# Performance work log

Measured on AMD Instinct MI355X. Metric: run time of the kernel, lower is better.

The kernel has to match this reference:

```python
import jax, jax.numpy as jnp
import numpy as np

E = 100   # embed_size
H = 64    # q_hidden_num
B, T, K = 64, 20, 50
I, U = 50000, 10000


def setup_inputs() -> dict:
    key = jax.random.key(0)
    ks = jax.random.split(key, 16)
    # sample_vectors: table = sigma[i]*randn + mu[i]; sigma=[1,1,1,.1,.1,1,1], mu=0
    alpha = jax.random.normal(ks[0], (I, E), jnp.float32)
    rho = jax.random.normal(ks[1], (I, E), jnp.float32)
    lam = jax.random.normal(ks[2], (I, E), jnp.float32)
    beta = 0.1 * jax.random.normal(ks[3], (I, E), jnp.float32)
    mu_tab = 0.1 * jax.random.normal(ks[4], (I, E), jnp.float32)
    theta = jax.random.normal(ks[5], (U, E), jnp.float32)
    gamma = jax.random.normal(ks[6], (U, E), jnp.float32)
    w1 = jax.random.normal(ks[7], (H, E), jnp.float32) / np.sqrt(E)
    b1 = jnp.zeros((H,), jnp.float32)
    w2 = jax.random.normal(ks[8], (1, H), jnp.float32) / np.sqrt(H)
    b2 = jnp.zeros((1,), jnp.float32)
    sigma_list = jnp.array([1.0, 1.0, 1.0, 0.1, 0.1, 1.0, 1.0], jnp.float32)
    mu_list = jnp.zeros((7,), jnp.float32)
    prices = jax.random.uniform(ks[9], (B, T), jnp.float32, 1.0, 20.0)
    price_table = jax.random.uniform(ks[10], (I,), jnp.float32, 1.0, 20.0)
    item_ids = jax.random.randint(ks[11], (B, T), 0, I, jnp.int32)
    # distinct itemset ids per row (contiguous random window)
    starts = jax.random.randint(ks[12], (B,), 0, I - K, jnp.int32)
    itemset = starts[:, None] + jnp.arange(K, dtype=jnp.int32)[None, :]
    userid = jax.random.randint(ks[13], (B,), 0, U, jnp.int32)
    return dict(alpha=alpha, rho=rho, lam=lam, beta=beta, mu_tab=mu_tab,
                theta=theta, gamma=gamma, w1=w1, b1=b1, w2=w2, b2=b2,
                sigma_list=sigma_list, mu_list=mu_list, prices=prices,
                price_table=price_table, item_ids=item_ids, itemset=itemset,
                userid=userid, batch_size=B)


def reference(alpha, rho, lam, beta, mu_tab, theta, gamma, w1, b1, w2, b2,
              sigma_list, mu_list, prices, price_table, item_ids, itemset,
              userid, batch_size):
    f32 = alpha.dtype

    def Qf(x):  # Q_function in eval mode (dropout identity)
        h = jax.nn.relu(x @ w1.T + b1)
        return jax.nn.sigmoid(h @ w2.T + b2)  # [..., 1]; mean over last dim == itself

    def prior_sum(v, idx):  # sum_e 0.5*(v-mu)*(-(v-mu)/sigma)
        return (-0.5 / sigma_list[idx]) * jnp.sum((v - mu_list[idx]) ** 2)

    th = theta[userid]   # [B,E]
    ga = gamma[userid]   # [B,E]
    a_c = alpha[itemset]; r_c = rho[itemset]; l_c = lam[itemset]
    b_c = beta[itemset]; m_c = mu_tab[itemset]          # [B,K,E]
    a0 = alpha[item_ids]; r0 = rho[item_ids]
    l0 = lam[item_ids]; b0 = beta[item_ids]             # [B,T,E]

    # ---- f prior ----
    q_l = (Qf(a_c).sum() + Qf(r_c).sum() + Qf(l_c).sum() + Qf(b_c).sum()
           + Qf(m_c).sum() + Qf(th).sum() + Qf(ga).sum())
    p_l = (prior_sum(a_c, 0) + prior_sum(r_c, 1) + prior_sum(l_c, 2)
           + prior_sum(b_c, 3) + prior_sum(m_c, 4)
           + prior_sum(th, 5) + prior_sum(ga, 6))

    # ---- kesai(item, user, price) ----
    def kes(a_i, b_i, l_i, th_b, ga_b, price):
        return (l_i.mean(-1) + (th_b * a_i).mean(-1)
                - (ga_b * b_i).mean(-1) * jnp.log(price))

    kes0 = kes(a0, b0, l0, th[:, None, :], ga[:, None, :], prices)            # [B,T]
    kesc = kes(a_c, b_c, l_c, th[:, None, :], ga[:, None, :], price_table[itemset])  # [B,K]

    # list-aliasing bug: basket at step k = [item0, c_0..c_k] (c_j skipped iff ==item0)
    m = itemset[:, None, :] != item_ids[:, :, None]     # [B,T,K]
    mf = m.astype(f32)
    S = a0[:, :, None, :] + jnp.cumsum(mf[..., None] * a_c[:, None, :, :], axis=2)  # [B,T,K,E]
    lenk = 1.0 + jnp.cumsum(mf, axis=2)                 # [B,T,K]

    D = jnp.einsum('btke,bje->btkj', S, r_c)            # rho_cj . S_k
    rda0 = jnp.einsum('bje,bte->btj', r_c, a0)          # rho_cj . alpha_item0
    A_kj = jnp.einsum('bke,bje->bkj', a_c, r_c)         # rho_cj . alpha_ck

    denom = (lenk + 1.0)[..., None] * E                 # [B,T,K,1]
    j_gt_k = jnp.arange(K)[:, None] < jnp.arange(K)[None, :]
    elig = m[:, :, None, :] & j_gt_k[None, None, :, :]  # [B,T,K,K]
    NEG = jnp.asarray(-1e30, f32)

    val0 = (D + rda0[:, :, None, :]) / denom + kesc[:, None, None, :]
    look0 = jnp.maximum(0.0, jnp.max(jnp.where(elig, val0, NEG), axis=-1))
    valc = (D + A_kj[:, None, :, :]) / denom + kesc[:, None, None, :]
    lookc = jnp.maximum(0.0, jnp.max(jnp.where(elig, valc, NEG), axis=-1))

    interact0 = jnp.einsum('bte,btke->btk', r0, S) / (E * lenk)
    interactc = jnp.einsum('bke,btke->btk', r_c, S) / (E * lenk)

    Kes0 = kes0[:, :, None] + interact0 + look0
    KesC = kesc[:, None, :] + interactc + lookc
    basket = jnp.sum(jnp.where(m, jax.nn.log_sigmoid(Kes0 - KesC), 0.0))

    # torch: loss = sum over batch; torch.mean(scalar) == scalar
    return p_l - q_l + basket
```

## Files before the change

### kernel.cpp

```cpp
#include <hip/hip_runtime.h>
#include <math.h>

#define Ee 100
#define Hh 64
#define Bb 64
#define Tt 20
#define Kk 50
#define NROWS (5*Bb*Kk + 2*Bb)
#define NQUADS (NROWS/4)
#define PREBLKS 256
#define QBLKS   512
#define NB3 (Bb*Tt)

__device__ __forceinline__ float wave_sum(float v) {
    #pragma unroll
    for (int m = 32; m >= 1; m >>= 1) v += __shfl_xor(v, m, 64);
    return v;
}
__device__ __forceinline__ float rl(float v, int l) {
    return __uint_as_float(__builtin_amdgcn_readlane(__float_as_uint(v), l));
}

__global__ __launch_bounds__(256) void k_fused1(
    const float* __restrict__ alpha, const float* __restrict__ rho,
    const float* __restrict__ lam,   const float* __restrict__ beta,
    const float* __restrict__ mu_tab,const float* __restrict__ theta,
    const float* __restrict__ gamma_,const float* __restrict__ w1,
    const float* __restrict__ b1,    const float* __restrict__ w2,
    const float* __restrict__ b2,    const float* __restrict__ sigma_list,
    const float* __restrict__ prices,const float* __restrict__ price_table,
    const int* __restrict__ item_ids,const int* __restrict__ itemset,
    const int* __restrict__ userid,
    float* __restrict__ A, float* __restrict__ rda0, float* __restrict__ ra0c,
    float* __restrict__ kesc, float* __restrict__ kes0, float* __restrict__ rda0self,
    float* __restrict__ partialQ)
{
    __shared__ float buf[12224];
    const int lane = threadIdx.x & 63;
    const int wid  = threadIdx.x >> 6;

    if (blockIdx.x < PREBLKS) {
        float* acT = buf;
        float* rcT = buf + 5200;
        float* a0T = buf + 10400;
        float* r0T = buf + 11200;
        float* th  = buf + 12000;
        float* ga  = buf + 12100;

        const int b = blockIdx.x >> 2, q = blockIdx.x & 3;
        const int kcnt = (q < 2) ? 13 : 12;
        const int kbeg = q*12 + ((q < 2) ? q : 2);
        const int tbeg = q*5;
        const long uid = userid[b];

        for (int i = threadIdx.x; i < Ee; i += 256) {
            th[i] = theta[uid*Ee+i];
            ga[i] = gamma_[uid*Ee+i];
        }
        for (int i = threadIdx.x; i < 2500; i += 256) {
            int ii = (i < 1250) ? i : i - 1250;
            int k = ii % 50, c = ii / 50;
            long idx = itemset[b*Kk+k];
            const float* src = ((i < 1250) ? alpha : rho) + idx*Ee + 4*c;
            float4 v = *(const float4*)src;
            float* dst = (i < 1250) ? acT : rcT;
            dst[(4*c+0)*52+k] = v.x; dst[(4*c+1)*52+k] = v.y;
            dst[(4*c+2)*52+k] = v.z; dst[(4*c+3)*52+k] = v.w;
        }
        for (int i = threadIdx.x; i < 250; i += 256) {
            int ii = (i < 125) ? i : i - 125;
            int tl = ii % 5, c = ii / 5;
            long idx = item_ids[b*Tt + tbeg + tl];
            const float* src = ((i < 125) ? alpha : rho) + idx*Ee + 4*c;
            float4 v = *(const float4*)src;
            float* dst = (i < 125) ? a0T : r0T;
            dst[(4*c+0)*8+tl] = v.x; dst[(4*c+1)*8+tl] = v.y;
            dst[(4*c+2)*8+tl] = v.z; dst[(4*c+3)*8+tl] = v.w;
        }
        __syncthreads();

        const int tid = threadIdx.x;
        if (tid < kcnt*13) {
            int k = kbeg + tid/13, jt = tid - (tid/13)*13, j0 = 4*jt;
            float s0=0.f, s1=0.f, s2=0.f, s3=0.f;
            #pragma unroll 4
            for (int e = 0; e < Ee; ++e) {
                float a  = acT[e*52 + k];
                float4 r = *(const float4*)&rcT[e*52 + j0];
                s0 = fmaf(a, r.x, s0); s1 = fmaf(a, r.y, s1);
                s2 = fmaf(a, r.z, s2); s3 = fmaf(a, r.w, s3);
            }
            float* dst = A + ((long)b*Kk + k)*Kk + j0;
            dst[0] = s0; dst[1] = s1;
            if (jt < 12) { dst[2] = s2; dst[3] = s3; }
        } else if (tid < kcnt*13 + 65) {
            int t2 = tid - kcnt*13;
            int tl = t2/13, jt = t2 - tl*13, j0 = 4*jt;
            float p0=0.f,p1=0.f,p2=0.f,p3=0.f, q0=0.f,q1=0.f,q2=0.f,q3=0.f;
            #pragma unroll 4
            for (int e = 0; e < Ee; ++e) {
                float a0v = a0T[e*8 + tl];
                float r0v = r0T[e*8 + tl];
                float4 r = *(const float4*)&rcT[e*52 + j0];
                float4 a = *(const float4*)&acT[e*52 + j0];
                p0 = fmaf(r.x, a0v, p0); p1 = fmaf(r.y, a0v, p1);
                p2 = fmaf(r.z, a0v, p2); p3 = fmaf(r.w, a0v, p3);
                q0 = fmaf(r0v, a.x, q0); q1 = fmaf(r0v, a.y, q1);
                q2 = fmaf(r0v, a.z, q2); q3 = fmaf(r0v, a.w, q3);
            }
            int t = tbeg + tl;
            float* d1 = rda0 + ((long)b*Tt + t)*Kk + j0;
            float* d2 = ra0c + ((long)b*Tt + t)*Kk + j0;
            d1[0]=p0; d1[1]=p1; d2[0]=q0; d2[1]=q1;
            if (jt < 12) { d1[2]=p2; d1[3]=p3; d2[2]=q2; d2[3]=q3; }
        }

        for (int task = wid; task < 5 + kcnt; task += 4) {
            if (task < 5) {
                int tl = task, t = tbeg + tl;
                long idx = item_ids[b*Tt+t];
                float s=0.f, ml=0.f, mtha=0.f, mgb=0.f;
                if (lane < Kk) {
                    #pragma unroll
                    for (int u = 0; u < 2; ++u) {
                        int e = lane + u*Kk;
                        float a0v = a0T[e*8+tl], r0v = r0T[e*8+tl];
                        s    = fmaf(r0v, a0v, s);
                        ml  += lam[idx*Ee+e];
                        mtha = fmaf(th[e], a0v, mtha);
                        mgb  = fmaf(ga[e], beta[idx*Ee+e], mgb);
                    }
                }
                s = wave_sum(s); ml = wave_sum(ml); mtha = wave_sum(mtha); mgb = wave_sum(mgb);
                if (lane == 0) {
                    rda0self[b*Tt+t] = s;
                    kes0[b*Tt+t] = 0.01f*ml + 0.01f*mtha - 0.01f*mgb*logf(prices[b*Tt+t]);
                }
            } else {
                int k = kbeg + (task - 5);
                long idx = itemset[b*Kk+k];
                float ml=0.f, mtha=0.f, mgb=0.f;
                if (lane < Kk) {
                    #pragma unroll
                    for (int u = 0; u < 2; ++u) {
                        int e = lane + u*Kk;
                        ml  += lam[idx*Ee+e];
                        mtha = fmaf(th[e], acT[e*52+k], mtha);
                        mgb  = fmaf(ga[e], beta[idx*Ee+e], mgb);
                    }
                }
                ml = wave_sum(ml); mtha = wave_sum(mtha); mgb = wave_sum(mgb);
                if (lane == 0)
                    kesc[b*Kk+k] = 0.01f*ml + 0.01f*mtha - 0.01f*mgb*logf(price_table[idx]);
            }
        }
    } else {
        float* w1s = buf;
        float* red = buf + 6400;

        for (int i = threadIdx.x; i < Hh*Ee/4; i += 256)
            *(float4*)&w1s[4*i] = *(const float4*)&w1[4*i];
        __syncthreads();

        const float w2j = w2[lane];
        const float b1j = b1[lane];
        const float b2v = b2[0];
        const float c0 = -0.5f/sigma_list[0], c1 = -0.5f/sigma_list[1];
        const float c2 = -0.5f/sigma_list[2], c3 = -0.5f/sigma_list[3];
        const float c4 = -0.5f/sigma_list[4], c5 = -0.5f/sigma_list[5];
        const float c6 = -0.5f/sigma_list[6];

        const bool ldA = (lane < 25);
        const bool ldB = (lane >= 32) && (lane < 57);
        const int  lq  = ldA ? (lane<<2) : ((lane-32)<<2);
        const int  wave = (blockIdx.x - PREBLKS)*4 + wid;

        #define LOAD_QUAD(Q, AB, CD, CF)                                          \
        {                                                                         \
            int r4_ = 4*(Q);                                                      \
            const float* tab_; int4 ii_;                                          \
            if (r4_ < 16000) {                                                    \
                int seg_ = r4_/3200;                                              \
                ii_ = *(const int4*)&itemset[r4_ - seg_*3200];                    \
                tab_ = (seg_==0)?alpha:(seg_==1)?rho:(seg_==2)?lam                \
                      :(seg_==3)?beta:mu_tab;                                     \
                CF = (seg_==0)?c0:(seg_==1)?c1:(seg_==2)?c2:(seg_==3)?c3:c4;      \
            } else if (r4_ < 16064) {                                             \
                ii_ = *(const int4*)&userid[r4_-16000]; tab_ = theta;  CF = c5;   \
            } else {                                                              \
                ii_ = *(const int4*)&userid[r4_-16064]; tab_ = gamma_; CF = c6;   \
            }                                                                     \
            if (ldA) {                                                            \
                AB = *(const float4*)(tab_ + (long)ii_.x*Ee + lq);                \
                CD = *(const float4*)(tab_ + (long)ii_.z*Ee + lq);                \
            } else if (ldB) {                                                     \
                AB = *(const float4*)(tab_ + (long)ii_.y*Ee + lq);                \
                CD = *(const float4*)(tab_ + (long)ii_.w*Ee + lq);                \
            }                                                                     \
        }

        float ssacc = 0.f;
        float qacc  = 0.f;
        float4 curAB = make_float4(0.f,0.f,0.f,0.f);
        float4 curCD = make_float4(0.f,0.f,0.f,0.f);
        float  ccur = 0.f;
        int qd = wave;
        if (qd < NQUADS) LOAD_QUAD(qd, curAB, curCD, ccur);

        while (qd < NQUADS) {
            float4 nAB = make_float4(0.f,0.f,0.f,0.f);
            float4 nCD = make_float4(0.f,0.f,0.f,0.f);
            float  cnx = 0.f;
            int qn = qd + QBLKS*4;
            if (qn < NQUADS) LOAD_QUAD(qn, nAB, nCD, cnx);

            if (ldA || ldB)
                ssacc += ccur * (curAB.x*curAB.x + curAB.y*curAB.y
                               + curAB.z*curAB.z + curAB.w*curAB.w
                               + curCD.x*curCD.x + curCD.y*curCD.y
                               + curCD.z*curCD.z + curCD.w*curCD.w);

            float hA0=b1j, hA1=0.f, hB0=b1j, hB1=0.f;
            float hC0=b1j, hC1=0.f, hD0=b1j, hD1=0.f;
            #pragma unroll
            for (int i = 0; i < 25; ++i) {
                float4 wv = *(const float4*)&w1s[lane*Ee + 4*i];
                hA0 = fmaf(rl(curAB.x, i),    wv.x, hA0);
                hA1 = fmaf(rl(curAB.y, i),    wv.y, hA1);
                hA0 = fmaf(rl(curAB.z, i),    wv.z, hA0);
                hA1 = fmaf(rl(curAB.w, i),    wv.w, hA1);
                hB0 = fmaf(rl(curAB.x, 32+i), wv.x, hB0);
                hB1 = fmaf(rl(curAB.y, 32+i), wv.y, hB1);
                hB0 = fmaf(rl(curAB.z, 32+i), wv.z, hB0);
                hB1 = fmaf(rl(curAB.w, 32+i), wv.w, hB1);
                hC0 = fmaf(rl(curCD.x, i),    wv.x, hC0);
                hC1 = fmaf(rl(curCD.y, i),    wv.y, hC1);
                hC0 = fmaf(rl(curCD.z, i),    wv.z, hC0);
                hC1 = fmaf(rl(curCD.w, i),    wv.w, hC1);
                hD0 = fmaf(rl(curCD.x, 32+i), wv.x, hD0);
                hD1 = fmaf(rl(curCD.y, 32+i), wv.y, hD1);
                hD0 = fmaf(rl(curCD.z, 32+i), wv.z, hD0);
                hD1 = fmaf(rl(curCD.w, 32+i), wv.w, hD1);
            }
            float vA = fmaxf(hA0+hA1, 0.f)*w2j;
            float vB = fmaxf(hB0+hB1, 0.f)*w2j;
            float vC = fmaxf(hC0+hC1, 0.f)*w2j;
            float vD = fmaxf(hD0+hD1, 0.f)*w2j;
            #pragma unroll
            for (int m = 32; m >= 1; m >>= 1) {
                vA += __shfl_xor(vA, m, 64);
                vB += __shfl_xor(vB, m, 64);
                vC += __shfl_xor(vC, m, 64);
                vD += __shfl_xor(vD, m, 64);
            }
            qacc -= 1.f/(1.f+expf(-(vA+b2v))) + 1.f/(1.f+expf(-(vB+b2v)))
                  + 1.f/(1.f+expf(-(vC+b2v))) + 1.f/(1.f+expf(-(vD+b2v)));

            curAB = nAB; curCD = nCD; ccur = cnx; qd = qn;
        }
        #undef LOAD_QUAD

        float s = wave_sum(ssacc);
        if (lane == 0) red[wid] = s + qacc;
        __syncthreads();
        if (threadIdx.x == 0)
            partialQ[blockIdx.x - PREBLKS] = red[0]+red[1]+red[2]+red[3];
    }
}

__global__ __launch_bounds__(64) void k_main(
    const float* __restrict__ A, const float* __restrict__ rda0,
    const float* __restrict__ ra0c, const float* __restrict__ kesc,
    const float* __restrict__ kes0, const float* __restrict__ rda0self,
    const int* __restrict__ item_ids, const int* __restrict__ itemset,
    float* __restrict__ partial)
{
    __shared__ float Als[Kk*51];
    __shared__ float Cum[Kk*51];
    __shared__ float2 js[Kk];

    const int bt = blockIdx.x;
    const int b  = bt / Tt;
    const int lane = threadIdx.x;

    for (int i = lane; i < Kk*Kk; i += 64) {
        int k = i / Kk;
        Als[k*51 + (i - k*Kk)] = A[(long)b*Kk*Kk + i];
    }

    const int  myitem = item_ids[bt];
    const bool valid  = lane < Kk;
    const int  cj     = valid ? itemset[b*Kk+lane] : -1;
    const bool mj     = valid && (cj != myitem);
    const unsigned long long mask = __ballot(mj);

    const float rj_own = valid ? rda0[(long)bt*Kk+lane] : 0.f;
    const float kc_own = valid ? kesc[b*Kk+lane] : 0.f;
    const float raj    = valid ? ra0c[(long)bt*Kk+lane] : 0.f;
    if (valid) js[lane] = make_float2(rj_own, kc_own);

    const unsigned mlo = (unsigned)mask, mhi = (unsigned)(mask >> 32);
    const int below = __builtin_amdgcn_mbcnt_hi(mhi, __builtin_amdgcn_mbcnt_lo(mlo, 0));
    const float len    = 1.f + (float)below + (mj ? 1.f : 0.f);
    const float invden = 1.f / ((len + 1.f) * (float)Ee);
    const float invlen = 1.f / ((float)Ee * len);

    float pv = mj ? raj : 0.f;
    #pragma unroll
    for (int off = 1; off <= 32; off <<= 1) {
        float u = __shfl_up(pv, off, 64);
        if (lane >= off) pv += u;
    }
    const float cumra  = pv;
    const float r0self = rda0self[bt];
    const float k0     = kes0[bt];

    asm volatile("s_waitcnt lgkmcnt(0)" ::: "memory");

    if (valid) {
        float cum = 0.f;
        #pragma unroll 5
        for (int k = 0; k < Kk; ++k) {
            float mfk = ((mask >> k) & 1ull) ? 1.0f : 0.0f;
            cum = fmaf(mfk, Als[k*51 + lane], cum);
            Cum[k*51 + lane] = cum;
        }
    }
    asm volatile("s_waitcnt lgkmcnt(0)" ::: "memory");

    const int lc = valid ? lane : (Kk-1);
    float max0 = -3e38f, maxc = -3e38f, diag = 0.f;
    #pragma unroll 2
    for (int j = 0; j < Kk; ++j) {
        float c = Cum[lc*51 + j];
        if (j == lane) diag = c;
        if ((mask >> j) & 1ull) {
            float  a  = Als[lc*51 + j];
            float2 sj = js[j];
            float v0 = fmaf(c + 2.f*sj.x, invden, sj.y);
            float vc = fmaf(a - sj.x,    invden, v0);
            if (lane < j) { max0 = fmaxf(max0, v0); maxc = fmaxf(maxc, vc); }
        }
    }

    float look0 = fmaxf(0.f, max0);
    float lookc = fmaxf(0.f, maxc);
    float Kes0 = k0     + fmaf(r0self + cumra, invlen, look0);
    float KesC = kc_own + fmaf(rj_own + diag,  invlen, lookc);
    float x = Kes0 - KesC;
    float term = (x >= 0.f) ? -log1pf(expf(-x)) : (x - log1pf(expf(x)));
    float contrib = mj ? term : 0.f;
    float s = wave_sum(contrib);
    if (lane == 0) partial[bt] = s;
}

__global__ __launch_bounds__(256) void k_final(
    const float* __restrict__ p1, int n1,
    const float* __restrict__ p3, int n3,
    float* __restrict__ out)
{
    __shared__ double sh[256];
    double s = 0.0;
    for (int i = threadIdx.x; i < n1; i += 256) s += (double)p1[i];
    for (int i = threadIdx.x; i < n3; i += 256) s += (double)p3[i];
    sh[threadIdx.x] = s;
    __syncthreads();
    for (int m = 128; m >= 1; m >>= 1) {
        if (threadIdx.x < m) sh[threadIdx.x] += sh[threadIdx.x + m];
        __syncthreads();
    }
    if (threadIdx.x == 0) out[0] = (float)sh[0];
}

extern "C" void kernel_launch(void* const* d_in, const int* in_sizes, int n_in,
                              void* d_out, int out_size, void* d_ws, size_t ws_size,
                              hipStream_t stream) {
    const float* alpha      = (const float*)d_in[0];
    const float* rho        = (const float*)d_in[1];
    const float* lam        = (const float*)d_in[2];
    const float* beta       = (const float*)d_in[3];
    const float* mu_tab     = (const float*)d_in[4];
    const float* theta      = (const float*)d_in[5];
    const float* gamma_     = (const float*)d_in[6];
    const float* w1         = (const float*)d_in[7];
    const float* b1         = (const float*)d_in[8];
    const float* w2         = (const float*)d_in[9];
    const float* b2         = (const float*)d_in[10];
    const float* sigma_list = (const float*)d_in[11];
    const float* prices      = (const float*)d_in[13];
    const float* price_table = (const float*)d_in[14];
    const int*   item_ids    = (const int*)d_in[15];
    const int*   itemset     = (const int*)d_in[16];
    const int*   userid      = (const int*)d_in[17];

    float* ws = (float*)d_ws;
    const size_t offA    = 0;
    const size_t offRDA  = offA   + (size_t)Bb*Kk*Kk;
    const size_t offRA0C = offRDA + (size_t)Bb*Tt*Kk;
    const size_t offKESC = offRA0C+ (size_t)Bb*Tt*Kk;
    const size_t offKES0 = offKESC+ (size_t)Bb*Kk;
    const size_t offSELF = offKES0+ (size_t)Bb*Tt;
    const size_t offP1   = offSELF+ (size_t)Bb*Tt;
    const size_t offP3   = offP1  + QBLKS;

    k_fused1<<<PREBLKS + QBLKS, 256, 0, stream>>>(
        alpha, rho, lam, beta, mu_tab, theta, gamma_,
        w1, b1, w2, b2, sigma_list, prices, price_table,
        item_ids, itemset, userid,
        ws + offA, ws + offRDA, ws + offRA0C,
        ws + offKESC, ws + offKES0, ws + offSELF,
        ws + offP1);
    k_main<<<NB3, 64, 0, stream>>>(ws + offA, ws + offRDA, ws + offRA0C,
                                   ws + offKESC, ws + offKES0, ws + offSELF,
                                   item_ids, itemset, ws + offP3);
    k_final<<<1, 256, 0, stream>>>(ws + offP1, QBLKS, ws + offP3, NB3, (float*)d_out);
}
```

Baseline: 36.41 us.

## Fuse basket stage into per-batch blocks, dropping k_main and global intermediates

```diff
diff --git a/kernel.cpp b/kernel.cpp
--- a/kernel.cpp
+++ b/kernel.cpp
@@ -6,11 +6,28 @@
 #define Bb 64
 #define Tt 20
 #define Kk 50
-#define NROWS (5*Bb*Kk + 2*Bb)
-#define NQUADS (NROWS/4)
-#define PREBLKS 256
-#define QBLKS   512
-#define NB3 (Bb*Tt)
+#define NROWS 16128
+#define NQUADS 4032
+#define BBLKS 64
+#define QBLKS 448
+#define NBLK (BBLKS + QBLKS)
+
+#define O_ACT   0
+#define O_RCT   5200
+#define O_P     5200
+#define O_W     7760
+#define O_ALS   10400
+#define O_RDA   12950
+#define O_RA0   13950
+#define O_KESC  14950
+#define O_KES0  15000
+#define O_SELF  15020
+#define O_TH    15040
+#define O_GA    15140
+#define O_IIS   15240
+#define O_IID   15292
+#define O_RED   15312
+#define LDSF    15320
 
 __device__ __forceinline__ float wave_sum(float v) {
     #pragma unroll
@@ -21,7 +38,7 @@
     return __uint_as_float(__builtin_amdgcn_readlane(__float_as_uint(v), l));
 }
 
-__global__ __launch_bounds__(256) void k_fused1(
+__global__ __launch_bounds__(256) void k_fused(
     const float* __restrict__ alpha, const float* __restrict__ rho,
     const float* __restrict__ lam,   const float* __restrict__ beta,
     const float* __restrict__ mu_tab,const float* __restrict__ theta,
@@ -31,134 +48,227 @@
     const float* __restrict__ prices,const float* __restrict__ price_table,
     const int* __restrict__ item_ids,const int* __restrict__ itemset,
     const int* __restrict__ userid,
-    float* __restrict__ A, float* __restrict__ rda0, float* __restrict__ ra0c,
-    float* __restrict__ kesc, float* __restrict__ kes0, float* __restrict__ rda0self,
-    float* __restrict__ partialQ)
+    float* __restrict__ partial)
 {
-    __shared__ float buf[12224];
-    const int lane = threadIdx.x & 63;
-    const int wid  = threadIdx.x >> 6;
-
-    if (blockIdx.x < PREBLKS) {
-        float* acT = buf;
-        float* rcT = buf + 5200;
-        float* a0T = buf + 10400;
-        float* r0T = buf + 11200;
-        float* th  = buf + 12000;
-        float* ga  = buf + 12100;
-
-        const int b = blockIdx.x >> 2, q = blockIdx.x & 3;
-        const int kcnt = (q < 2) ? 13 : 12;
-        const int kbeg = q*12 + ((q < 2) ? q : 2);
-        const int tbeg = q*5;
-        const long uid = userid[b];
-
-        for (int i = threadIdx.x; i < Ee; i += 256) {
-            th[i] = theta[uid*Ee+i];
-            ga[i] = gamma_[uid*Ee+i];
-        }
-        for (int i = threadIdx.x; i < 2500; i += 256) {
-            int ii = (i < 1250) ? i : i - 1250;
-            int k = ii % 50, c = ii / 50;
-            long idx = itemset[b*Kk+k];
-            const float* src = ((i < 1250) ? alpha : rho) + idx*Ee + 4*c;
-            float4 v = *(const float4*)src;
-            float* dst = (i < 1250) ? acT : rcT;
+    __shared__ float buf[LDSF];
+    const int tid  = threadIdx.x;
+    const int lane = tid & 63;
+    const int wid  = tid >> 6;
+
+    if (blockIdx.x < BBLKS) {
+        const int b = blockIdx.x;
+        int* iis = (int*)&buf[O_IIS];
+        int* iid = (int*)&buf[O_IID];
+
+        if (tid < Kk) iis[tid] = itemset[b*Kk + tid];
+        else if (tid < Kk + Tt) iid[tid - Kk] = item_ids[b*Tt + (tid - Kk)];
+        {
+            const long uid = userid[b];
+            if (tid >= 64 && tid < 89)
+                *(float4*)&buf[O_TH + 4*(tid-64)] = *(const float4*)&theta[uid*Ee + 4*(tid-64)];
+            else if (tid >= 96 && tid < 121)
+                *(float4*)&buf[O_GA + 4*(tid-96)] = *(const float4*)&gamma_[uid*Ee + 4*(tid-96)];
+        }
+        for (int i = tid; i < 2500; i += 256) {
+            int half = (i < 1250) ? 0 : 1;
+            int ii = i - half*1250;
+            int k = ii % Kk, c = ii / Kk;
+            long idx = itemset[b*Kk + k];
+            float4 v = *(const float4*)((half ? rho : alpha) + idx*Ee + 4*c);
+            float* dst = &buf[half ? O_RCT : O_ACT];
             dst[(4*c+0)*52+k] = v.x; dst[(4*c+1)*52+k] = v.y;
             dst[(4*c+2)*52+k] = v.z; dst[(4*c+3)*52+k] = v.w;
         }
-        for (int i = threadIdx.x; i < 250; i += 256) {
-            int ii = (i < 125) ? i : i - 125;
-            int tl = ii % 5, c = ii / 5;
-            long idx = item_ids[b*Tt + tbeg + tl];
-            const float* src = ((i < 125) ? alpha : rho) + idx*Ee + 4*c;
-            float4 v = *(const float4*)src;
-            float* dst = (i < 125) ? a0T : r0T;
-            dst[(4*c+0)*8+tl] = v.x; dst[(4*c+1)*8+tl] = v.y;
-            dst[(4*c+2)*8+tl] = v.z; dst[(4*c+3)*8+tl] = v.w;
-        }
-        __syncthreads();
-
-        const int tid = threadIdx.x;
-        if (tid < kcnt*13) {
-            int k = kbeg + tid/13, jt = tid - (tid/13)*13, j0 = 4*jt;
-            float s0=0.f, s1=0.f, s2=0.f, s3=0.f;
-            #pragma unroll 4
-            for (int e = 0; e < Ee; ++e) {
-                float a  = acT[e*52 + k];
-                float4 r = *(const float4*)&rcT[e*52 + j0];
-                s0 = fmaf(a, r.x, s0); s1 = fmaf(a, r.y, s1);
-                s2 = fmaf(a, r.z, s2); s3 = fmaf(a, r.w, s3);
-            }
-            float* dst = A + ((long)b*Kk + k)*Kk + j0;
-            dst[0] = s0; dst[1] = s1;
-            if (jt < 12) { dst[2] = s2; dst[3] = s3; }
-        } else if (tid < kcnt*13 + 65) {
-            int t2 = tid - kcnt*13;
-            int tl = t2/13, jt = t2 - tl*13, j0 = 4*jt;
-            float p0=0.f,p1=0.f,p2=0.f,p3=0.f, q0=0.f,q1=0.f,q2=0.f,q3=0.f;
-            #pragma unroll 4
-            for (int e = 0; e < Ee; ++e) {
-                float a0v = a0T[e*8 + tl];
-                float r0v = r0T[e*8 + tl];
-                float4 r = *(const float4*)&rcT[e*52 + j0];
-                float4 a = *(const float4*)&acT[e*52 + j0];
-                p0 = fmaf(r.x, a0v, p0); p1 = fmaf(r.y, a0v, p1);
-                p2 = fmaf(r.z, a0v, p2); p3 = fmaf(r.w, a0v, p3);
-                q0 = fmaf(r0v, a.x, q0); q1 = fmaf(r0v, a.y, q1);
-                q2 = fmaf(r0v, a.z, q2); q3 = fmaf(r0v, a.w, q3);
-            }
-            int t = tbeg + tl;
-            float* d1 = rda0 + ((long)b*Tt + t)*Kk + j0;
-            float* d2 = ra0c + ((long)b*Tt + t)*Kk + j0;
-            d1[0]=p0; d1[1]=p1; d2[0]=q0; d2[1]=q1;
-            if (jt < 12) { d1[2]=p2; d1[3]=p3; d2[2]=q2; d2[3]=q3; }
-        }
-
-        for (int task = wid; task < 5 + kcnt; task += 4) {
-            if (task < 5) {
-                int tl = task, t = tbeg + tl;
-                long idx = item_ids[b*Tt+t];
-                float s=0.f, ml=0.f, mtha=0.f, mgb=0.f;
-                if (lane < Kk) {
+        __syncthreads();
+
+        for (int task = tid; task < 369; task += 256) {
+            if (task < 169) {
+                int kt = task / 13, jt = task - 13*(task/13);
+                int k0 = 4*kt, j0 = 4*jt;
+                float acc[4][4] = {};
+                #pragma unroll 4
+                for (int e = 0; e < Ee; ++e) {
+                    float4 a4 = *(const float4*)&buf[O_ACT + e*52 + k0];
+                    float4 r4 = *(const float4*)&buf[O_RCT + e*52 + j0];
+                    acc[0][0]=fmaf(a4.x,r4.x,acc[0][0]); acc[0][1]=fmaf(a4.x,r4.y,acc[0][1]);
+                    acc[0][2]=fmaf(a4.x,r4.z,acc[0][2]); acc[0][3]=fmaf(a4.x,r4.w,acc[0][3]);
+                    acc[1][0]=fmaf(a4.y,r4.x,acc[1][0]); acc[1][1]=fmaf(a4.y,r4.y,acc[1][1]);
+                    acc[1][2]=fmaf(a4.y,r4.z,acc[1][2]); acc[1][3]=fmaf(a4.y,r4.w,acc[1][3]);
+                    acc[2][0]=fmaf(a4.z,r4.x,acc[2][0]); acc[2][1]=fmaf(a4.z,r4.y,acc[2][1]);
+                    acc[2][2]=fmaf(a4.z,r4.z,acc[2][2]); acc[2][3]=fmaf(a4.z,r4.w,acc[2][3]);
+                    acc[3][0]=fmaf(a4.w,r4.x,acc[3][0]); acc[3][1]=fmaf(a4.w,r4.y,acc[3][1]);
+                    acc[3][2]=fmaf(a4.w,r4.z,acc[3][2]); acc[3][3]=fmaf(a4.w,r4.w,acc[3][3]);
+                }
+                int km = Kk - k0; if (km > 4) km = 4;
+                int jm = Kk - j0; if (jm > 4) jm = 4;
+                #pragma unroll
+                for (int a = 0; a < 4; ++a)
                     #pragma unroll
-                    for (int u = 0; u < 2; ++u) {
-                        int e = lane + u*Kk;
-                        float a0v = a0T[e*8+tl], r0v = r0T[e*8+tl];
-                        s    = fmaf(r0v, a0v, s);
-                        ml  += lam[idx*Ee+e];
-                        mtha = fmaf(th[e], a0v, mtha);
-                        mgb  = fmaf(ga[e], beta[idx*Ee+e], mgb);
-                    }
+                    for (int c2 = 0; c2 < 4; ++c2)
+                        if (a < km && c2 < jm)
+                            buf[O_ALS + (k0+a)*51 + (j0+c2)] = acc[a][c2];
+            } else if (task < 299) {
+                int t2 = task - 169;
+                int tt = t2 / 13, jt = t2 - 13*tt;
+                int t0 = 2*tt, j0 = 4*jt;
+                long ia0 = iid[t0], ia1 = iid[t0+1];
+                const float *a0p0 = alpha + ia0*Ee, *r0p0 = rho + ia0*Ee;
+                const float *a0p1 = alpha + ia1*Ee, *r0p1 = rho + ia1*Ee;
+                float p0[4]={},p1[4]={},q0[4]={},q1[4]={};
+                for (int c = 0; c < 25; ++c) {
+                    float4 av0 = *(const float4*)(a0p0 + 4*c);
+                    float4 av1 = *(const float4*)(a0p1 + 4*c);
+                    float4 rv0 = *(const float4*)(r0p0 + 4*c);
+                    float4 rv1 = *(const float4*)(r0p1 + 4*c);
+                    #define RDA_STEP(d, comp)                                               \
+                    {   float4 rc4 = *(const float4*)&buf[O_RCT + (4*c+d)*52 + j0];         \
+                        float4 ac4 = *(const float4*)&buf[O_ACT + (4*c+d)*52 + j0];         \
+                        p0[0]=fmaf(rc4.x,av0.comp,p0[0]); p0[1]=fmaf(rc4.y,av0.comp,p0[1]); \
+                        p0[2]=fmaf(rc4.z,av0.comp,p0[2]); p0[3]=fmaf(rc4.w,av0.comp,p0[3]); \
+                        p1[0]=fmaf(rc4.x,av1.comp,p1[0]); p1[1]=fmaf(rc4.y,av1.comp,p1[1]); \
+                        p1[2]=fmaf(rc4.z,av1.comp,p1[2]); p1[3]=fmaf(rc4.w,av1.comp,p1[3]); \
+                        q0[0]=fmaf(rv0.comp,ac4.x,q0[0]); q0[1]=fmaf(rv0.comp,ac4.y,q0[1]); \
+                        q0[2]=fmaf(rv0.comp,ac4.z,q0[2]); q0[3]=fmaf(rv0.comp,ac4.w,q0[3]); \
+                        q1[0]=fmaf(rv1.comp,ac4.x,q1[0]); q1[1]=fmaf(rv1.comp,ac4.y,q1[1]); \
+                        q1[2]=fmaf(rv1.comp,ac4.z,q1[2]); q1[3]=fmaf(rv1.comp,ac4.w,q1[3]); }
+                    RDA_STEP(0,x) RDA_STEP(1,y) RDA_STEP(2,z) RDA_STEP(3,w)
+                    #undef RDA_STEP
                 }
-                s = wave_sum(s); ml = wave_sum(ml); mtha = wave_sum(mtha); mgb = wave_sum(mgb);
-                if (lane == 0) {
-                    rda0self[b*Tt+t] = s;
-                    kes0[b*Tt+t] = 0.01f*ml + 0.01f*mtha - 0.01f*mgb*logf(prices[b*Tt+t]);
+                int jm = Kk - j0; if (jm > 4) jm = 4;
+                #pragma unroll
+                for (int jj = 0; jj < 4; ++jj) if (jj < jm) {
+                    buf[O_RDA + t0*50 + j0+jj] = p0[jj];
+                    buf[O_RDA + (t0+1)*50 + j0+jj] = p1[jj];
+                    buf[O_RA0 + t0*50 + j0+jj] = q0[jj];
+                    buf[O_RA0 + (t0+1)*50 + j0+jj] = q1[jj];
                 }
+            } else if (task < 349) {
+                int k = task - 299;
+                long idx = iis[k];
+                const float *lp = lam + idx*Ee, *bp = beta + idx*Ee;
+                float ml=0.f, mtha=0.f, mgb=0.f;
+                for (int c = 0; c < 25; ++c) {
+                    float4 l4 = *(const float4*)(lp + 4*c);
+                    float4 b4 = *(const float4*)(bp + 4*c);
+                    float4 t4 = *(const float4*)&buf[O_TH + 4*c];
+                    float4 g4 = *(const float4*)&buf[O_GA + 4*c];
+                    ml  += (l4.x + l4.y) + (l4.z + l4.w);
+                    mgb += g4.x*b4.x + g4.y*b4.y + g4.z*b4.z + g4.w*b4.w;
+                    float a0 = buf[O_ACT + (4*c+0)*52 + k];
+                    float a1 = buf[O_ACT + (4*c+1)*52 + k];
+                    float a2 = buf[O_ACT + (4*c+2)*52 + k];
+                    float a3 = buf[O_ACT + (4*c+3)*52 + k];
+                    mtha += t4.x*a0 + t4.y*a1 + t4.z*a2 + t4.w*a3;
+                }
+                buf[O_KESC + k] = 0.01f*(ml + mtha) - 0.01f*mgb*logf(price_table[idx]);
             } else {
-                int k = kbeg + (task - 5);
-                long idx = itemset[b*Kk+k];
-                float ml=0.f, mtha=0.f, mgb=0.f;
-                if (lane < Kk) {
-                    #pragma unroll
-                    for (int u = 0; u < 2; ++u) {
-                        int e = lane + u*Kk;
-                        ml  += lam[idx*Ee+e];
-                        mtha = fmaf(th[e], acT[e*52+k], mtha);
-                        mgb  = fmaf(ga[e], beta[idx*Ee+e], mgb);
-                    }
+                int t = task - 349;
+                long ia = iid[t];
+                const float *ap = alpha + ia*Ee, *rp = rho + ia*Ee;
+                const float *lp = lam + ia*Ee,  *bp = beta + ia*Ee;
+                float self=0.f, ml=0.f, mtha=0.f, mgb=0.f;
+                for (int c = 0; c < 25; ++c) {
+                    float4 a4 = *(const float4*)(ap + 4*c);
+                    float4 r4 = *(const float4*)(rp + 4*c);
+                    float4 l4 = *(const float4*)(lp + 4*c);
+                    float4 b4 = *(const float4*)(bp + 4*c);
+                    float4 t4 = *(const float4*)&buf[O_TH + 4*c];
+                    float4 g4 = *(const float4*)&buf[O_GA + 4*c];
+                    self += a4.x*r4.x + a4.y*r4.y + a4.z*r4.z + a4.w*r4.w;
+                    ml   += (l4.x + l4.y) + (l4.z + l4.w);
+                    mtha += t4.x*a4.x + t4.y*a4.y + t4.z*a4.z + t4.w*a4.w;
+                    mgb  += g4.x*b4.x + g4.y*b4.y + g4.z*b4.z + g4.w*b4.w;
                 }
-                ml = wave_sum(ml); mtha = wave_sum(mtha); mgb = wave_sum(mgb);
-                if (lane == 0)
-                    kesc[b*Kk+k] = 0.01f*ml + 0.01f*mtha - 0.01f*mgb*logf(price_table[idx]);
-            }
-        }
+                buf[O_SELF + t] = self;
+                buf[O_KES0 + t] = 0.01f*(ml + mtha) - 0.01f*mgb*logf(prices[b*Tt + t]);
+            }
+        }
+        __syncthreads();
+
+        if (wid == 0 && lane < Kk) {
+            float s = 0.f;
+            #pragma unroll 5
+            for (int k = 0; k < Kk; ++k) {
+                s += buf[O_ALS + k*51 + lane];
+                buf[O_P + k*51 + lane] = s;
+            }
+        }
+        __syncthreads();
+
+        const int lc = (lane < Kk) ? lane : 0;
+        float PR[Kk], AR[Kk];
+        #pragma unroll
+        for (int j = 0; j < Kk; ++j) {
+            PR[j] = buf[O_P   + lc*51 + j];
+            AR[j] = buf[O_ALS + lc*51 + j];
+        }
+
+        float bacc = 0.f;
+        float* Wp = &buf[O_W + wid*208];
+        for (int it = 0; it < 5; ++it) {
+            const int t = wid*5 + it;
+            const int item = iid[t];
+            bool eq = (lane < Kk) && (iis[lane] == item);
+            unsigned long long mq = __ballot(eq);
+            int p_t = mq ? (int)__ffsll((long long)mq) - 1 : -1;
+
+            float raj = (lane < Kk) ? buf[O_RA0 + t*50 + lane] : 0.f;
+            float rj  = (lane < Kk) ? buf[O_RDA + t*50 + lane] : 0.f;
+            float pv = raj;
+            #pragma unroll
+            for (int off = 1; off <= 32; off <<= 1) {
+                float u = __shfl_up(pv, off, 64);
+                if (lane >= off) pv += u;
+            }
+            float rasub = (p_t >= 0) ? rl(raj, p_t) : 0.f;
+            float cumra = pv - ((p_t >= 0 && lane >= p_t) ? rasub : 0.f);
+
+            if (lane < Kk) {
+                float4 w;
+                w.x = rj;
+                w.y = buf[O_KESC + lane];
+                w.z = buf[O_ALS + (p_t < 0 ? 0 : p_t)*51 + lane];
+                w.w = 0.f;
+                *(float4*)&Wp[4*lane] = w;
+            }
+            int sub_le = (p_t >= 0 && p_t <= lane) ? 1 : 0;
+            float len = (float)(lane + 2 - sub_le);
+            float invden = 1.f / ((len + 1.f) * 100.f);
+            float invlen = 1.f / (100.f * len);
+            float subf = (p_t >= 0 && lane >= p_t) ? 1.f : 0.f;
+            asm volatile("s_waitcnt lgkmcnt(0)" ::: "memory");
+
+            float max0 = -3e38f, maxc = -3e38f, diag = 0.f;
+            #pragma unroll
+            for (int j = 0; j < Kk; ++j) {
+                float4 w = *(const float4*)&Wp[4*j];
+                float Cum = fmaf(-subf, w.z, PR[j]);
+                float base = Cum + w.x;
+                float v0 = fmaf(base + w.x, invden, w.y);
+                float vc = fmaf(base + AR[j], invden, w.y);
+                bool elig = (j > lane) && (j != p_t);
+                max0 = elig ? fmaxf(max0, v0) : max0;
+                maxc = elig ? fmaxf(maxc, vc) : maxc;
+                if (j == lane) diag = Cum;
+            }
+            float Kes0 = buf[O_KES0 + t]
+                       + fmaf(buf[O_SELF + t] + cumra, invlen, fmaxf(0.f, max0));
+            float KesC = buf[O_KESC + lc]
+                       + fmaf(rj + diag, invlen, fmaxf(0.f, maxc));
+            float x = Kes0 - KesC;
+            float term = (x >= 0.f) ? -log1pf(expf(-x)) : (x - log1pf(expf(x)));
+            if (lane < Kk && lane != p_t) bacc += term;
+        }
+        float s = wave_sum(bacc);
+        if (lane == 0) buf[O_RED + wid] = s;
+        __syncthreads();
+        if (tid == 0)
+            partial[b] = buf[O_RED] + buf[O_RED+1] + buf[O_RED+2] + buf[O_RED+3];
     } else {
         float* w1s = buf;
         float* red = buf + 6400;
 
-        for (int i = threadIdx.x; i < Hh*Ee/4; i += 256)
+        for (int i = tid; i < Hh*Ee/4; i += 256)
             *(float4*)&w1s[4*i] = *(const float4*)&w1[4*i];
         __syncthreads();
 
@@ -173,7 +283,7 @@
         const bool ldA = (lane < 25);
         const bool ldB = (lane >= 32) && (lane < 57);
         const int  lq  = ldA ? (lane<<2) : ((lane-32)<<2);
-        const int  wave = (blockIdx.x - PREBLKS)*4 + wid;
+        const int  wave = (blockIdx.x - BBLKS)*4 + wid;
 
         #define LOAD_QUAD(Q, AB, CD, CF)                                          \
         {                                                                         \
@@ -199,8 +309,7 @@
             }                                                                     \
         }
 
-        float ssacc = 0.f;
-        float qacc  = 0.f;
+        float ssacc = 0.f, qacc = 0.f;
         float4 curAB = make_float4(0.f,0.f,0.f,0.f);
         float4 curCD = make_float4(0.f,0.f,0.f,0.f);
         float  ccur = 0.f;
@@ -263,106 +372,17 @@
         float s = wave_sum(ssacc);
         if (lane == 0) red[wid] = s + qacc;
         __syncthreads();
-        if (threadIdx.x == 0)
-            partialQ[blockIdx.x - PREBLKS] = red[0]+red[1]+red[2]+red[3];
+        if (tid == 0)
+            partial[blockIdx.x] = red[0]+red[1]+red[2]+red[3];
     }
 }
 
-__global__ __launch_bounds__(64) void k_main(
-    const float* __restrict__ A, const float* __restrict__ rda0,
-    const float* __restrict__ ra0c, const float* __restrict__ kesc,
-    const float* __restrict__ kes0, const float* __restrict__ rda0self,
-    const int* __restrict__ item_ids, const int* __restrict__ itemset,
-    float* __restrict__ partial)
-{
-    __shared__ float Als[Kk*51];
-    __shared__ float Cum[Kk*51];
-    __shared__ float2 js[Kk];
-
-    const int bt = blockIdx.x;
-    const int b  = bt / Tt;
-    const int lane = threadIdx.x;
-
-    for (int i = lane; i < Kk*Kk; i += 64) {
-        int k = i / Kk;
-        Als[k*51 + (i - k*Kk)] = A[(long)b*Kk*Kk + i];
-    }
-
-    const int  myitem = item_ids[bt];
-    const bool valid  = lane < Kk;
-    const int  cj     = valid ? itemset[b*Kk+lane] : -1;
-    const bool mj     = valid && (cj != myitem);
-    const unsigned long long mask = __ballot(mj);
-
-    const float rj_own = valid ? rda0[(long)bt*Kk+lane] : 0.f;
-    const float kc_own = valid ? kesc[b*Kk+lane] : 0.f;
-    const float raj    = valid ? ra0c[(long)bt*Kk+lane] : 0.f;
-    if (valid) js[lane] = make_float2(rj_own, kc_own);
-
-    const unsigned mlo = (unsigned)mask, mhi = (unsigned)(mask >> 32);
-    const int below = __builtin_amdgcn_mbcnt_hi(mhi, __builtin_amdgcn_mbcnt_lo(mlo, 0));
-    const float len    = 1.f + (float)below + (mj ? 1.f : 0.f);
-    const float invden = 1.f / ((len + 1.f) * (float)Ee);
-    const float invlen = 1.f / ((float)Ee * len);
-
-    float pv = mj ? raj : 0.f;
-    #pragma unroll
-    for (int off = 1; off <= 32; off <<= 1) {
-        float u = __shfl_up(pv, off, 64);
-        if (lane >= off) pv += u;
-    }
-    const float cumra  = pv;
-    const float r0self = rda0self[bt];
-    const float k0     = kes0[bt];
-
-    asm volatile("s_waitcnt lgkmcnt(0)" ::: "memory");
-
-    if (valid) {
-        float cum = 0.f;
-        #pragma unroll 5
-        for (int k = 0; k < Kk; ++k) {
-            float mfk = ((mask >> k) & 1ull) ? 1.0f : 0.0f;
-            cum = fmaf(mfk, Als[k*51 + lane], cum);
-            Cum[k*51 + lane] = cum;
-        }
-    }
-    asm volatile("s_waitcnt lgkmcnt(0)" ::: "memory");
-
-    const int lc = valid ? lane : (Kk-1);
-    float max0 = -3e38f, maxc = -3e38f, diag = 0.f;
-    #pragma unroll 2
-    for (int j = 0; j < Kk; ++j) {
-        float c = Cum[lc*51 + j];
-        if (j == lane) diag = c;
-        if ((mask >> j) & 1ull) {
-            float  a  = Als[lc*51 + j];
-            float2 sj = js[j];
-            float v0 = fmaf(c + 2.f*sj.x, invden, sj.y);
-            float vc = fmaf(a - sj.x,    invden, v0);
-            if (lane < j) { max0 = fmaxf(max0, v0); maxc = fmaxf(maxc, vc); }
-        }
-    }
-
-    float look0 = fmaxf(0.f, max0);
-    float lookc = fmaxf(0.f, maxc);
-    float Kes0 = k0     + fmaf(r0self + cumra, invlen, look0);
-    float KesC = kc_own + fmaf(rj_own + diag,  invlen, lookc);
-    float x = Kes0 - KesC;
-    float term = (x >= 0.f) ? -log1pf(expf(-x)) : (x - log1pf(expf(x)));
-    float contrib = mj ? term : 0.f;
-    float s = wave_sum(contrib);
-    if (lane == 0) partial[bt] = s;
-}
-
 __global__ __launch_bounds__(256) void k_final(
-    const float* __restrict__ p1, int n1,
-    const float* __restrict__ p3, int n3,
-    float* __restrict__ out)
+    const float* __restrict__ p, int n, float* __restrict__ out)
 {
     __shared__ double sh[256];
     double s = 0.0;
-    for (int i = threadIdx.x; i < n1; i += 256) s += (double)p1[i];
-    for (int i = threadIdx.x; i < n3; i += 256) s += (double)p3[i];
+    for (int i = threadIdx.x; i < n; i += 256) s += (double)p[i];
     sh[threadIdx.x] = s;
     __syncthreads();
     for (int m = 128; m >= 1; m >>= 1) {
@@ -394,24 +414,10 @@
     const int*   userid      = (const int*)d_in[17];
 
     float* ws = (float*)d_ws;
-    const size_t offA    = 0;
-    const size_t offRDA  = offA   + (size_t)Bb*Kk*Kk;
-    const size_t offRA0C = offRDA + (size_t)Bb*Tt*Kk;
-    const size_t offKESC = offRA0C+ (size_t)Bb*Tt*Kk;
-    const size_t offKES0 = offKESC+ (size_t)Bb*Kk;
-    const size_t offSELF = offKES0+ (size_t)Bb*Tt;
-    const size_t offP1   = offSELF+ (size_t)Bb*Tt;
-    const size_t offP3   = offP1  + QBLKS;
-
-    k_fused1<<<PREBLKS + QBLKS, 256, 0, stream>>>(
+
+    k_fused<<<NBLK, 256, 0, stream>>>(
         alpha, rho, lam, beta, mu_tab, theta, gamma_,
         w1, b1, w2, b2, sigma_list, prices, price_table,
-        item_ids, itemset, userid,
-        ws + offA, ws + offRDA, ws + offRA0C,
-        ws + offKESC, ws + offKES0, ws + offSELF,
-        ws + offP1);
-    k_main<<<NB3, 64, 0, stream>>>(ws + offA, ws + offRDA, ws + offRA0C,
-                                   ws + offKESC, ws + offKES0, ws + offSELF,
-                                   item_ids, itemset, ws + offP3);
-    k_final<<<1, 256, 0, stream>>>(ws + offP1, QBLKS, ws + offP3, NB3, (float*)d_out);
+        item_ids, itemset, userid, ws);
+    k_final<<<1, 256, 0, stream>>>(ws, NBLK, (float*)d_out);
 }
```

Result: slower. 40.97 us (+12.6%).
